# Kernel tuning notes

Measured on AMD Instinct MI355X. Metric: run time of the kernel, lower is better.

The kernel has to match this reference:

```python
import jax, jax.numpy as jnp
import numpy as np

H = 8          # head_num
DK = 16        # qkv_dim
CLIP = 10.0    # logit clipping


def _heads(x):
    # (b, n, H*DK) -> (b, H, n, DK)
    b, n, _ = x.shape
    return x.reshape(b, n, H, DK).transpose(0, 2, 1, 3)


def setup_inputs() -> dict:
    key = jax.random.key(0)
    ks = jax.random.split(key, 10)
    batch, problem, d, klen = 2048, 100, 128, 10
    s = 1.0 / np.sqrt(d)
    problems = jax.random.uniform(ks[0], (batch, problem, 2), dtype=jnp.float32)
    encoded_nodes = jax.random.normal(ks[1], (batch, problem, d), dtype=jnp.float32)
    Wq_first = jax.random.normal(ks[2], (d, H * DK), dtype=jnp.float32) * s
    Wq_last = jax.random.normal(ks[3], (d, H * DK), dtype=jnp.float32) * s
    Wk = jax.random.normal(ks[4], (d, H * DK), dtype=jnp.float32) * s
    Wv = jax.random.normal(ks[5], (d, H * DK), dtype=jnp.float32) * s
    Wcomb = jax.random.normal(ks[6], (H * DK, d), dtype=jnp.float32) * s
    # prefix: k distinct node indices per batch row (first k of a random permutation)
    perm = jax.vmap(lambda kk: jax.random.permutation(kk, problem))(
        jax.random.split(ks[7], batch))
    prefix = perm[:, :klen].astype(jnp.int32)
    return {"problems": problems, "encoded_nodes": encoded_nodes,
            "Wq_first": Wq_first, "Wq_last": Wq_last, "Wk": Wk, "Wv": Wv,
            "Wcomb": Wcomb, "prefix": prefix}


def reference(problems, encoded_nodes, Wq_first, Wq_last, Wk, Wv, Wcomb, prefix):
    batch, problem, d = encoded_nodes.shape
    b_idx = jnp.arange(batch)
    sqrt_dk = jnp.sqrt(jnp.float32(DK))
    sqrt_d = jnp.sqrt(jnp.float32(d))

    # set_kv: precompute multi-head K, V once (single-head key = encoded_nodes)
    kh = _heads(encoded_nodes @ Wk)   # (b, H, n, DK)
    vh = _heads(encoded_nodes @ Wv)   # (b, H, n, DK)

    # set_q1: query contribution of the first node (last node of prefix)
    last0 = prefix[:, -1]
    q1 = _heads(encoded_nodes[b_idx, last0][:, None, :] @ Wq_first)  # (b, H, 1, DK)

    # visited mask from prefix
    visited0 = jnp.zeros((batch, problem), dtype=bool)
    visited0 = visited0.at[b_idx[:, None], prefix].set(True)

    def step(carry, _):
        visited, cur = carry
        enc_last = encoded_nodes[b_idx, cur][:, None, :]            # (b, 1, d)
        q = q1 + _heads(enc_last @ Wq_last)                         # (b, H, 1, DK)
        ninf = jnp.where(visited, -jnp.inf, 0.0)                    # (b, n)
        scores = jnp.einsum('bhqe,bhne->bhqn', q, kh) / sqrt_dk
        att = jax.nn.softmax(scores + ninf[:, None, None, :], axis=-1)
        mh = jnp.einsum('bhqn,bhne->bhqe', att, vh)                 # (b, H, 1, DK)
        mh = mh.transpose(0, 2, 1, 3).reshape(batch, 1, H * DK) @ Wcomb  # (b, 1, d)
        sc = jnp.einsum('bqd,bnd->bqn', mh, encoded_nodes)[:, 0] / sqrt_d  # (b, n)
        logits = CLIP * jnp.tanh(sc) + ninf
        sel = jnp.argmax(logits, axis=-1)                           # (b,)
        visited = visited.at[b_idx, sel].set(True)
        return (visited, sel), sel

    steps = problem - prefix.shape[1]
    _, sels = jax.lax.scan(step, (visited0, last0), None, length=steps)
    tour = jnp.concatenate([prefix, sels.T.astype(prefix.dtype)], axis=1)  # (b, problem)
    return tour
```

## Files before the change

### kernel.cpp

```cpp
#include <hip/hip_runtime.h>
#include <math.h>

#define N      100
#define D      128
#define H      8
#define DKH    16
#define KL     10
#define S0     90
#define STEPS  90
#define SROWS  48
#define LDK    132
#define NT     512

__device__ __forceinline__ float dot4(float4 a, float4 b) {
  return a.x*b.x + a.y*b.y + a.z*b.z + a.w*b.w;
}
__device__ __forceinline__ void fma4(float4& acc, float a, float4 v) {
  acc.x += a*v.x; acc.y += a*v.y; acc.z += a*v.z; acc.w += a*v.w;
}

__device__ __forceinline__ void compute_chunk(const float* __restrict__ encB,
                                              const float* __restrict__ W,
                                              bool wRowMajor, int base, int cnt,
                                              const int* __restrict__ slotNode,
                                              float* __restrict__ stage, int tid) {
  const int col = tid & 127;
  const int grp = tid >> 7;
  float acc[12];
  int   nd [12];
  #pragma unroll
  for (int ii = 0; ii < 12; ++ii) {
    acc[ii] = 0.f;
    int r = grp + 4*ii;
    nd[ii] = (r < cnt) ? __builtin_amdgcn_readfirstlane(slotNode[base + r]) : 0;
  }
  for (int dd = 0; dd < D; dd += 16) {
    float w[16];
    #pragma unroll
    for (int t = 0; t < 16; ++t)
      w[t] = wRowMajor ? W[col*D + dd + t] : W[(dd+t)*D + col];
    #pragma unroll
    for (int ii = 0; ii < 12; ++ii) {
      int r = grp + 4*ii;
      if (r < cnt) {
        const float* er = encB + (size_t)nd[ii]*D + dd;
        float a0=0,a1=0,a2=0,a3=0;
        #pragma unroll
        for (int t = 0; t < 16; t += 4) {
          a0 += er[t]*w[t];   a1 += er[t+1]*w[t+1];
          a2 += er[t+2]*w[t+2]; a3 += er[t+3]*w[t+3];
        }
        acc[ii] += (a0+a1)+(a2+a3);
      }
    }
  }
  #pragma unroll
  for (int ii = 0; ii < 12; ++ii) {
    int r = grp + 4*ii;
    if (r < cnt) stage[r*LDK + col] = acc[ii];
  }
}

__global__ __launch_bounds__(NT, 4)
void policy_kernel(const float* __restrict__ enc,
                   const float* __restrict__ Wq_first,
                   const float* __restrict__ Wq_last,
                   const float* __restrict__ Wk,
                   const float* __restrict__ Wv,
                   const float* __restrict__ Wcomb,
                   const int*   __restrict__ prefix,
                   int*         __restrict__ out) {
  __shared__ __align__(16) float sQL[(S0+1)*D];
  __shared__ __align__(16) float sStage[SROWS*LDK];
  __shared__ __align__(16) float sAtt[H*96];
  __shared__ __align__(16) float sMh[D];
  __shared__ float sSum[H];
  __shared__ int   sSlotNode[96];
  __shared__ unsigned long long sPacked;
  __shared__ int   sLast0;

  const int tid = threadIdx.x;
  const int b   = blockIdx.x;
  const float* encB = enc + (size_t)b*N*D;

  if (tid < KL) out[(size_t)b*N + tid] = prefix[b*KL + tid];
  if (tid < 48) sAtt[(tid/6)*96 + 90 + (tid%6)] = 0.f;
  if (tid == 0) {
    unsigned vis[4] = {0u,0u,0u,0u};
    const int* pr = prefix + b*KL;
    for (int j = 0; j < KL; ++j) { int n = pr[j]; vis[n>>5] |= 1u << (n&31); }
    int cnt = 0;
    for (int n = 0; n < N; ++n)
      if (!((vis[n>>5] >> (n&31)) & 1u)) sSlotNode[cnt++] = n;
    sLast0  = pr[KL-1];
    sPacked = 0ull;
  }
  __syncthreads();

  if (tid < D) {
    const int last0 = sLast0;
    const float* er = encB + (size_t)last0*D;
    float a0=0,a1=0,a2=0,a3=0;
    #pragma unroll
    for (int d = 0; d < D; d += 4) {
      a0 += er[d]  *Wq_first[d*D     + tid];
      a1 += er[d+1]*Wq_first[(d+1)*D + tid];
      a2 += er[d+2]*Wq_first[(d+2)*D + tid];
      a3 += er[d+3]*Wq_first[(d+3)*D + tid];
    }
    sMh[tid] = (a0+a1)+(a2+a3);
  }
  __syncthreads();

  {
    const int col = tid & 127;
    const int grp = tid >> 7;
    float acc[23];
    int   nd [23];
    #pragma unroll
    for (int ii = 0; ii < 23; ++ii) {
      acc[ii] = 0.f;
      int r = grp + 4*ii;
      nd[ii] = (r < S0) ? __builtin_amdgcn_readfirstlane(sSlotNode[r])
                        : ((r == S0) ? sLast0 : 0);
    }
    for (int dd = 0; dd < D; dd += 16) {
      float w[16];
      #pragma unroll
      for (int t = 0; t < 16; ++t) w[t] = Wq_last[(dd+t)*D + col];
      #pragma unroll
      for (int ii = 0; ii < 23; ++ii) {
        int r = grp + 4*ii;
        if (r <= S0) {
          const float* er = encB + (size_t)nd[ii]*D + dd;
          float a0=0,a1=0,a2=0,a3=0;
          #pragma unroll
          for (int t = 0; t < 16; t += 4) {
            a0 += er[t]*w[t];   a1 += er[t+1]*w[t+1];
            a2 += er[t+2]*w[t+2]; a3 += er[t+3]*w[t+3];
          }
          acc[ii] += (a0+a1)+(a2+a3);
        }
      }
    }
    const float q1c = sMh[col];
    #pragma unroll
    for (int ii = 0; ii < 23; ++ii) {
      int r = grp + 4*ii;
      if (r <= S0) sQL[r*D + col] = acc[ii] + q1c;
    }
  }
  __syncthreads();

  const int h     = tid >> 6;
  const int l     = tid & 63;
  const int cQuad = tid >> 4;
  const int cStrm = tid & 15;
  const int di    = tid >> 2;
  const int dkc   = tid & 3;

  float4 ka0,ka1,ka2,ka3, kb0,kb1,kb2,kb3;
  compute_chunk(encB, Wk, false, 0, 48, sSlotNode, sStage, tid);
  __syncthreads();
  if (l < 48) {
    const float* p = &sStage[l*LDK + h*DKH];
    ka0 = *(const float4*)(p+0);  ka1 = *(const float4*)(p+4);
    ka2 = *(const float4*)(p+8);  ka3 = *(const float4*)(p+12);
  }
  __syncthreads();
  compute_chunk(encB, Wk, false, 48, 42, sSlotNode, sStage, tid);
  __syncthreads();
  if (l >= 48) {
    const float* p = &sStage[(l-48)*LDK + h*DKH];
    ka0 = *(const float4*)(p+0);  ka1 = *(const float4*)(p+4);
    ka2 = *(const float4*)(p+8);  ka3 = *(const float4*)(p+12);
  }
  if (l < 26) {
    const float* p = &sStage[(l+16)*LDK + h*DKH];
    kb0 = *(const float4*)(p+0);  kb1 = *(const float4*)(p+4);
    kb2 = *(const float4*)(p+8);  kb3 = *(const float4*)(p+12);
  } else {
    kb0=kb1=kb2=kb3 = make_float4(0.f,0.f,0.f,0.f);
  }
  __syncthreads();

  float4 v0,v1,v2,v3,v4,v5;
  compute_chunk(encB, Wv, false, 0, 48, sSlotNode, sStage, tid);
  __syncthreads();
  v0 = *(const float4*)&sStage[(cStrm     )*LDK + cQuad*4];
  v1 = *(const float4*)&sStage[(cStrm + 16)*LDK + cQuad*4];
  v2 = *(const float4*)&sStage[(cStrm + 32)*LDK + cQuad*4];
  __syncthreads();
  compute_chunk(encB, Wv, false, 48, 42, sSlotNode, sStage, tid);
  __syncthreads();
  v3 = *(const float4*)&sStage[(cStrm     )*LDK + cQuad*4];
  v4 = *(const float4*)&sStage[(cStrm + 16)*LDK + cQuad*4];
  v5 = (cStrm < 10) ? *(const float4*)&sStage[(cStrm + 32)*LDK + cQuad*4]
                    : make_float4(0.f,0.f,0.f,0.f);
  __syncthreads();

  float4 ce[8];
  compute_chunk(encB, Wcomb, true, 0, 48, sSlotNode, sStage, tid);
  __syncthreads();
  if (di < 48) {
    #pragma unroll
    for (int j = 0; j < 8; ++j)
      ce[j] = *(const float4*)&sStage[di*LDK + dkc*32 + j*4];
  }
  __syncthreads();
  compute_chunk(encB, Wcomb, true, 48, 42, sSlotNode, sStage, tid);
  __syncthreads();
  if (di >= 48 && di < S0) {
    #pragma unroll
    for (int j = 0; j < 8; ++j)
      ce[j] = *(const float4*)&sStage[(di-48)*LDK + dkc*32 + j*4];
  }
  __syncthreads();

  float visA = 0.f, visB = 0.f, visD = 0.f;
  int   curRow = S0;

  for (int step = 0; step < STEPS; ++step) {
    if (step > 0) {
      const unsigned long long u = sPacked;
      const int idx = 127 - (int)(u & 0xFFull);
      if (tid == 0) out[(size_t)b*N + KL + step - 1] = sSlotNode[idx];
      curRow = idx;
      if (idx == l)      visA = -INFINITY;
      if (idx == l + 64) visB = -INFINITY;
      if (idx == di)     visD = -INFINITY;
    }

    {
      const float* qr = &sQL[curRow*D + h*DKH];
      const float4 q0 = *(const float4*)(qr+0);
      const float4 q1 = *(const float4*)(qr+4);
      const float4 q2 = *(const float4*)(qr+8);
      const float4 q3 = *(const float4*)(qr+12);
      float s0 = dot4(q0,ka0)+dot4(q1,ka1)+dot4(q2,ka2)+dot4(q3,ka3);
      float x0 = expf(s0*0.25f + visA);
      sAtt[h*96 + l] = x0;
      float x1 = 0.f;
      if (l < 26) {
        float s1 = dot4(q0,kb0)+dot4(q1,kb1)+dot4(q2,kb2)+dot4(q3,kb3);
        x1 = expf(s1*0.25f + visB);
        sAtt[h*96 + 64 + l] = x1;
      }
      float loc = x0 + x1;
      #pragma unroll
      for (int off = 32; off; off >>= 1) loc += __shfl_xor(loc, off);
      if (l == 0) sSum[h] = loc;
    }
    __syncthreads();

    {
      if (tid == 0) sPacked = 0ull;
      const int ch = cQuad >> 2;
      float4 acc = make_float4(0.f,0.f,0.f,0.f);
      fma4(acc, sAtt[ch*96 + cStrm     ], v0);
      fma4(acc, sAtt[ch*96 + cStrm + 16], v1);
      fma4(acc, sAtt[ch*96 + cStrm + 32], v2);
      fma4(acc, sAtt[ch*96 + cStrm + 48], v3);
      fma4(acc, sAtt[ch*96 + cStrm + 64], v4);
      fma4(acc, sAtt[ch*96 + cStrm + 80], v5);
      #pragma unroll
      for (int off = 1; off < 16; off <<= 1) {
        acc.x += __shfl_xor(acc.x, off);
        acc.y += __shfl_xor(acc.y, off);
        acc.z += __shfl_xor(acc.z, off);
        acc.w += __shfl_xor(acc.w, off);
      }
      if (cStrm == 0) {
        const float r = 1.0f / sSum[ch];
        float4 o; o.x = acc.x*r; o.y = acc.y*r; o.z = acc.z*r; o.w = acc.w*r;
        *(float4*)&sMh[cQuad*4] = o;
      }
    }
    __syncthreads();

    if (tid < 384) {
      float a = 0.f;
      #pragma unroll
      for (int j = 0; j < 8; ++j) {
        const float4 mh = *(const float4*)&sMh[dkc*32 + j*4];
        a += dot4(ce[j], mh);
      }
      a += __shfl_xor(a, 1);
      a += __shfl_xor(a, 2);
      float val = (di < S0) ? a + visD : -INFINITY;
      int   idx = (di < S0) ? di : 127;
      #pragma unroll
      for (int off = 32; off; off >>= 1) {
        float ov = __shfl_xor(val, off);
        int   oi = __shfl_xor(idx, off);
        if (ov > val || (ov == val && oi < idx)) { val = ov; idx = oi; }
      }
      if (l == 0) {
        unsigned s = __float_as_uint(val);
        s = (s & 0x80000000u) ? ~s : (s | 0x80000000u);
        unsigned long long pk = ((unsigned long long)s << 32)
                              | (unsigned long long)(unsigned)(127 - idx);
        atomicMax(&sPacked, pk);
      }
    }
    __syncthreads();
  }

  if (tid == 0) {
    const unsigned long long u = sPacked;
    const int idx = 127 - (int)(u & 0xFFull);
    out[(size_t)b*N + KL + STEPS - 1] = sSlotNode[idx];
  }
}

extern "C" void kernel_launch(void* const* d_in, const int* in_sizes, int n_in,
                              void* d_out, int out_size, void* d_ws, size_t ws_size,
                              hipStream_t stream) {
  const float* enc      = (const float*)d_in[1];
  const float* Wq_first = (const float*)d_in[2];
  const float* Wq_last  = (const float*)d_in[3];
  const float* Wk       = (const float*)d_in[4];
  const float* Wv       = (const float*)d_in[5];
  const float* Wcomb    = (const float*)d_in[6];
  const int*   prefix   = (const int*)d_in[7];
  const int batch = in_sizes[7] / KL;
  policy_kernel<<<batch, NT, 0, stream>>>(enc, Wq_first, Wq_last, Wk, Wv, Wcomb,
                                          prefix, (int*)d_out);
}
```

Before: 2.557 ms.

## Keep query rows in registers and Wcomb projection in LDS instead

Drops the large per-row query table in shared memory. Each thread now keeps its 23 projected query values in registers and writes the selected row into a small shared buffer after every step, which adds one more barrier per step. The Wcomb-projected encodings move from registers to an LDS table read in every step, and the K/V/Wcomb staging into a full-size shared buffer removes several intermediate barriers. A double-buffered packed argmax slot lets the reset and the read of the selection happen without a race. This trades register pressure for LDS traffic and aims to change occupancy, at the cost of an extra synchronization per step.

```diff
diff --git a/kernel.cpp b/kernel.cpp
--- a/kernel.cpp
+++ b/kernel.cpp
@@ -3,12 +3,9 @@
 
 #define N      100
 #define D      128
-#define H      8
-#define DKH    16
 #define KL     10
 #define S0     90
 #define STEPS  90
-#define SROWS  48
 #define LDK    132
 #define NT     512
 
@@ -19,17 +16,18 @@
   acc.x += a*v.x; acc.y += a*v.y; acc.z += a*v.z; acc.w += a*v.w;
 }
 
-__device__ __forceinline__ void compute_chunk(const float* __restrict__ encB,
-                                              const float* __restrict__ W,
-                                              bool wRowMajor, int base, int cnt,
-                                              const int* __restrict__ slotNode,
-                                              float* __restrict__ stage, int tid) {
+template<int RPT>
+__device__ __forceinline__ void cc(const float* __restrict__ encB,
+                                   const float* __restrict__ W,
+                                   bool wRowMajor, int base, int cnt,
+                                   const int* __restrict__ slotNode,
+                                   float* __restrict__ stage, int tid) {
   const int col = tid & 127;
   const int grp = tid >> 7;
-  float acc[12];
-  int   nd [12];
+  float acc[RPT];
+  int   nd [RPT];
   #pragma unroll
-  for (int ii = 0; ii < 12; ++ii) {
+  for (int ii = 0; ii < RPT; ++ii) {
     acc[ii] = 0.f;
     int r = grp + 4*ii;
     nd[ii] = (r < cnt) ? __builtin_amdgcn_readfirstlane(slotNode[base + r]) : 0;
@@ -40,7 +38,7 @@
     for (int t = 0; t < 16; ++t)
       w[t] = wRowMajor ? W[col*D + dd + t] : W[(dd+t)*D + col];
     #pragma unroll
-    for (int ii = 0; ii < 12; ++ii) {
+    for (int ii = 0; ii < RPT; ++ii) {
       int r = grp + 4*ii;
       if (r < cnt) {
         const float* er = encB + (size_t)nd[ii]*D + dd;
@@ -55,9 +53,9 @@
     }
   }
   #pragma unroll
-  for (int ii = 0; ii < 12; ++ii) {
+  for (int ii = 0; ii < RPT; ++ii) {
     int r = grp + 4*ii;
-    if (r < cnt) stage[r*LDK + col] = acc[ii];
+    if (r < cnt) stage[(base + r)*LDK + col] = acc[ii];
   }
 }
 
@@ -70,13 +68,13 @@
                    const float* __restrict__ Wcomb,
                    const int*   __restrict__ prefix,
                    int*         __restrict__ out) {
-  __shared__ __align__(16) float sQL[(S0+1)*D];
-  __shared__ __align__(16) float sStage[SROWS*LDK];
-  __shared__ __align__(16) float sAtt[H*96];
+  __shared__ __align__(16) float sCE[S0*LDK];
+  __shared__ __align__(16) float sq[D];
+  __shared__ __align__(16) float sAtt[8*96];
   __shared__ __align__(16) float sMh[D];
-  __shared__ float sSum[H];
+  __shared__ float sSum[8];
   __shared__ int   sSlotNode[96];
-  __shared__ unsigned long long sPacked;
+  __shared__ unsigned long long sPacked[2];
   __shared__ int   sLast0;
 
   const int tid = threadIdx.x;
@@ -92,8 +90,8 @@
     int cnt = 0;
     for (int n = 0; n < N; ++n)
       if (!((vis[n>>5] >> (n&31)) & 1u)) sSlotNode[cnt++] = n;
-    sLast0  = pr[KL-1];
-    sPacked = 0ull;
+    sLast0 = pr[KL-1];
+    sPacked[0] = 0ull; sPacked[1] = 0ull;
   }
   __syncthreads();
 
@@ -112,17 +110,17 @@
   }
   __syncthreads();
 
+  const int col = tid & 127;
+  const int grp = tid >> 7;
+  float qp[23];
   {
-    const int col = tid & 127;
-    const int grp = tid >> 7;
-    float acc[23];
-    int   nd [23];
+    int nd[23];
     #pragma unroll
     for (int ii = 0; ii < 23; ++ii) {
-      acc[ii] = 0.f;
       int r = grp + 4*ii;
       nd[ii] = (r < S0) ? __builtin_amdgcn_readfirstlane(sSlotNode[r])
                         : ((r == S0) ? sLast0 : 0);
+      qp[ii] = 0.f;
     }
     for (int dd = 0; dd < D; dd += 16) {
       float w[16];
@@ -139,44 +137,27 @@
             a0 += er[t]*w[t];   a1 += er[t+1]*w[t+1];
             a2 += er[t+2]*w[t+2]; a3 += er[t+3]*w[t+3];
           }
-          acc[ii] += (a0+a1)+(a2+a3);
+          qp[ii] += (a0+a1)+(a2+a3);
         }
       }
     }
     const float q1c = sMh[col];
     #pragma unroll
-    for (int ii = 0; ii < 23; ++ii) {
-      int r = grp + 4*ii;
-      if (r <= S0) sQL[r*D + col] = acc[ii] + q1c;
-    }
-  }
-  __syncthreads();
-
-  const int h     = tid >> 6;
-  const int l     = tid & 63;
-  const int cQuad = tid >> 4;
-  const int cStrm = tid & 15;
-  const int di    = tid >> 2;
-  const int dkc   = tid & 3;
-
+    for (int ii = 0; ii < 23; ++ii) qp[ii] += q1c;
+  }
+
+  const int h = tid >> 6, l = tid & 63;
+
+  cc<23>(encB, Wk, false, 0, S0, sSlotNode, sCE, tid);
+  __syncthreads();
   float4 ka0,ka1,ka2,ka3, kb0,kb1,kb2,kb3;
-  compute_chunk(encB, Wk, false, 0, 48, sSlotNode, sStage, tid);
-  __syncthreads();
-  if (l < 48) {
-    const float* p = &sStage[l*LDK + h*DKH];
+  {
+    const float* p = &sCE[l*LDK + h*16];
     ka0 = *(const float4*)(p+0);  ka1 = *(const float4*)(p+4);
     ka2 = *(const float4*)(p+8);  ka3 = *(const float4*)(p+12);
   }
-  __syncthreads();
-  compute_chunk(encB, Wk, false, 48, 42, sSlotNode, sStage, tid);
-  __syncthreads();
-  if (l >= 48) {
-    const float* p = &sStage[(l-48)*LDK + h*DKH];
-    ka0 = *(const float4*)(p+0);  ka1 = *(const float4*)(p+4);
-    ka2 = *(const float4*)(p+8);  ka3 = *(const float4*)(p+12);
-  }
   if (l < 26) {
-    const float* p = &sStage[(l+16)*LDK + h*DKH];
+    const float* p = &sCE[(64+l)*LDK + h*16];
     kb0 = *(const float4*)(p+0);  kb1 = *(const float4*)(p+4);
     kb2 = *(const float4*)(p+8);  kb3 = *(const float4*)(p+12);
   } else {
@@ -184,59 +165,42 @@
   }
   __syncthreads();
 
+  const int cQuad = tid >> 4;
+  const int cStrm = tid & 15;
+  const int ch    = cQuad >> 2;
+  cc<12>(encB, Wv, false,  0, 48, sSlotNode, sCE, tid);
+  cc<12>(encB, Wv, false, 48, 42, sSlotNode, sCE, tid);
+  __syncthreads();
   float4 v0,v1,v2,v3,v4,v5;
-  compute_chunk(encB, Wv, false, 0, 48, sSlotNode, sStage, tid);
-  __syncthreads();
-  v0 = *(const float4*)&sStage[(cStrm     )*LDK + cQuad*4];
-  v1 = *(const float4*)&sStage[(cStrm + 16)*LDK + cQuad*4];
-  v2 = *(const float4*)&sStage[(cStrm + 32)*LDK + cQuad*4];
-  __syncthreads();
-  compute_chunk(encB, Wv, false, 48, 42, sSlotNode, sStage, tid);
-  __syncthreads();
-  v3 = *(const float4*)&sStage[(cStrm     )*LDK + cQuad*4];
-  v4 = *(const float4*)&sStage[(cStrm + 16)*LDK + cQuad*4];
-  v5 = (cStrm < 10) ? *(const float4*)&sStage[(cStrm + 32)*LDK + cQuad*4]
+  v0 = *(const float4*)&sCE[(cStrm     )*LDK + cQuad*4];
+  v1 = *(const float4*)&sCE[(cStrm + 16)*LDK + cQuad*4];
+  v2 = *(const float4*)&sCE[(cStrm + 32)*LDK + cQuad*4];
+  v3 = *(const float4*)&sCE[(cStrm + 48)*LDK + cQuad*4];
+  v4 = *(const float4*)&sCE[(cStrm + 64)*LDK + cQuad*4];
+  v5 = (cStrm < 10) ? *(const float4*)&sCE[(cStrm + 80)*LDK + cQuad*4]
                     : make_float4(0.f,0.f,0.f,0.f);
   __syncthreads();
 
-  float4 ce[8];
-  compute_chunk(encB, Wcomb, true, 0, 48, sSlotNode, sStage, tid);
-  __syncthreads();
-  if (di < 48) {
-    #pragma unroll
-    for (int j = 0; j < 8; ++j)
-      ce[j] = *(const float4*)&sStage[di*LDK + dkc*32 + j*4];
-  }
-  __syncthreads();
-  compute_chunk(encB, Wcomb, true, 48, 42, sSlotNode, sStage, tid);
-  __syncthreads();
-  if (di >= 48 && di < S0) {
-    #pragma unroll
-    for (int j = 0; j < 8; ++j)
-      ce[j] = *(const float4*)&sStage[(di-48)*LDK + dkc*32 + j*4];
-  }
-  __syncthreads();
-
+  cc<6>(encB, Wcomb, true,  0, 24, sSlotNode, sCE, tid);
+  cc<6>(encB, Wcomb, true, 24, 24, sSlotNode, sCE, tid);
+  cc<6>(encB, Wcomb, true, 48, 24, sSlotNode, sCE, tid);
+  cc<6>(encB, Wcomb, true, 72, 18, sSlotNode, sCE, tid);
+  if (grp == 2) sq[col] = qp[22];
+  __syncthreads();
+
+  const int di  = tid >> 2;
+  const int dkc = tid & 3;
   float visA = 0.f, visB = 0.f, visD = 0.f;
-  int   curRow = S0;
 
   for (int step = 0; step < STEPS; ++step) {
-    if (step > 0) {
-      const unsigned long long u = sPacked;
-      const int idx = 127 - (int)(u & 0xFFull);
-      if (tid == 0) out[(size_t)b*N + KL + step - 1] = sSlotNode[idx];
-      curRow = idx;
-      if (idx == l)      visA = -INFINITY;
-      if (idx == l + 64) visB = -INFINITY;
-      if (idx == di)     visD = -INFINITY;
-    }
+    const int p = step & 1;
 
     {
-      const float* qr = &sQL[curRow*D + h*DKH];
-      const float4 q0 = *(const float4*)(qr+0);
-      const float4 q1 = *(const float4*)(qr+4);
-      const float4 q2 = *(const float4*)(qr+8);
-      const float4 q3 = *(const float4*)(qr+12);
+      if (tid == NT-1) sPacked[p] = 0ull;
+      const float4 q0 = *(const float4*)&sq[h*16 + 0];
+      const float4 q1 = *(const float4*)&sq[h*16 + 4];
+      const float4 q2 = *(const float4*)&sq[h*16 + 8];
+      const float4 q3 = *(const float4*)&sq[h*16 + 12];
       float s0 = dot4(q0,ka0)+dot4(q1,ka1)+dot4(q2,ka2)+dot4(q3,ka3);
       float x0 = expf(s0*0.25f + visA);
       sAtt[h*96 + l] = x0;
@@ -254,8 +218,6 @@
     __syncthreads();
 
     {
-      if (tid == 0) sPacked = 0ull;
-      const int ch = cQuad >> 2;
       float4 acc = make_float4(0.f,0.f,0.f,0.f);
       fma4(acc, sAtt[ch*96 + cStrm     ], v0);
       fma4(acc, sAtt[ch*96 + cStrm + 16], v1);
@@ -272,7 +234,7 @@
       }
       if (cStrm == 0) {
         const float r = 1.0f / sSum[ch];
-        float4 o; o.x = acc.x*r; o.y = acc.y*r; o.z = acc.z*r; o.w = acc.w*r;
+        float4 o; o.x=acc.x*r; o.y=acc.y*r; o.z=acc.z*r; o.w=acc.w*r;
         *(float4*)&sMh[cQuad*4] = o;
       }
     }
@@ -282,8 +244,9 @@
       float a = 0.f;
       #pragma unroll
       for (int j = 0; j < 8; ++j) {
+        const float4 ce = *(const float4*)&sCE[di*LDK + dkc*32 + j*4];
         const float4 mh = *(const float4*)&sMh[dkc*32 + j*4];
-        a += dot4(ce[j], mh);
+        a += dot4(ce, mh);
       }
       a += __shfl_xor(a, 1);
       a += __shfl_xor(a, 2);
@@ -300,16 +263,25 @@
         s = (s & 0x80000000u) ? ~s : (s | 0x80000000u);
         unsigned long long pk = ((unsigned long long)s << 32)
                               | (unsigned long long)(unsigned)(127 - idx);
-        atomicMax(&sPacked, pk);
+        atomicMax(&sPacked[p], pk);
       }
     }
     __syncthreads();
-  }
-
-  if (tid == 0) {
-    const unsigned long long u = sPacked;
-    const int idx = 127 - (int)(u & 0xFFull);
-    out[(size_t)b*N + KL + STEPS - 1] = sSlotNode[idx];
+
+    {
+      const unsigned long long u = sPacked[p];
+      const int idx = __builtin_amdgcn_readfirstlane(127 - (int)(u & 0xFFull));
+      if (tid == 0) out[(size_t)b*N + KL + step] = sSlotNode[idx];
+      if (idx == l)      visA = -INFINITY;
+      if (idx == l + 64) visB = -INFINITY;
+      if (idx == di)     visD = -INFINITY;
+      const int want = idx >> 2;
+      float qv = qp[0];
+      #pragma unroll
+      for (int ii = 1; ii < 23; ++ii) qv = (want == ii) ? qp[ii] : qv;
+      if (grp == (idx & 3)) sq[col] = qv;
+    }
+    __syncthreads();
   }
 }
 
```

New measurement: 2.546 ms. No clear change (-0.4%).
